# Performance work log

Measured on AMD Instinct MI355X. Metric: run time of the kernel, lower is better.

Reference implementation:

```python
import jax, jax.numpy as jnp
import numpy as np
import math

B, S, D, H = 2, 2048, 1024, 16
HD = D // H  # head_dim = 64


def setup_inputs() -> dict:
    key = jax.random.key(0)
    k1, k2, k3, k4, k5 = jax.random.split(key, 5)
    scale_in = 1.0 / math.sqrt(D)
    return {
        "x": jax.random.normal(k1, (B, S, D), dtype=jnp.float32),
        "Wqkv": jax.random.normal(k2, (3 * D, D), dtype=jnp.float32) * scale_in,
        "bqkv": jax.random.normal(k3, (3 * D,), dtype=jnp.float32) * 0.01,
        "Wout": jax.random.normal(k4, (D, D), dtype=jnp.float32) * scale_in,
        "bout": jax.random.normal(k5, (D,), dtype=jnp.float32) * 0.01,
    }


def reference(x, Wqkv, bqkv, Wout, bout):
    Bs, Sl, Dm = x.shape
    # qkv projection: torch Linear is x @ W.T + b
    qkv = x @ Wqkv.T + bqkv                        # [B,S,3D]
    qkv = qkv.reshape(Bs, Sl, 3, H, HD)
    q, k, v = qkv[:, :, 0], qkv[:, :, 1], qkv[:, :, 2]  # each [B,S,H,d]
    softmax_scale = 1.0 / math.sqrt(HD)
    # NOTE: source einsum 'bshd,btjd->bsht' sums k over its head axis j.
    # Equivalent efficient form: pre-sum k (and v) over heads.
    k_sum = k.sum(axis=2)                          # [B,S,d]
    v_sum = v.sum(axis=2)                          # [B,S,d]
    scores = jnp.einsum('bshd,btd->bsht', q, k_sum) * softmax_scale  # [B,S,H,T]
    causal_mask = jnp.triu(jnp.ones((Sl, Sl), dtype=bool), k=1)      # [S,T]
    scores = jnp.where(causal_mask[None, :, None, :], -jnp.inf, scores)
    attn = jax.nn.softmax(scores, axis=-1)
    # dropout p=0.0 / eval mode -> identity
    out = jnp.einsum('bsht,btd->bshd', attn, v_sum)  # [B,S,H,d]
    out = out.reshape(Bs, Sl, Dm)
    return out @ Wout.T + bout
```

## Files before the change

kernel.cpp:

```cpp
#include <hip/hip_runtime.h>


#define S_LEN 2048
#define DIM 1024

using floatx4 = __attribute__((ext_vector_type(4))) float;
using halfx8  = __attribute__((ext_vector_type(8))) _Float16;
using halfx4  = __attribute__((ext_vector_type(4))) _Float16;

__device__ __forceinline__ floatx4 mfma16(halfx8 a, halfx8 b, floatx4 c) {
  return __builtin_amdgcn_mfma_f32_16x16x32_f16(a, b, c, 0, 0, 0);
}

__device__ __forceinline__ void gll16(const void* g, void* l) {
  __builtin_amdgcn_global_load_lds(
      (const __attribute__((address_space(1))) void*)g,
      (__attribute__((address_space(3))) void*)l, 16, 0, 0);
}

__global__ __launch_bounds__(256) void prep_all(
    const float* __restrict__ x, const float* __restrict__ wqkv,
    const float* __restrict__ bqkv, const float* __restrict__ wout,
    _Float16* __restrict__ xb, _Float16* __restrict__ wcomb,
    _Float16* __restrict__ woutb, float* __restrict__ bcomb) {
  int bx = blockIdx.x;
  if (bx < 6144) {
    size_t i4 = ((size_t)bx * 256 + threadIdx.x) * 4;
    const float* src;
    _Float16* dst;
    size_t off;
    if (i4 < 4194304) { src = x; dst = xb; off = i4; }
    else if (i4 < 5242880) { src = wqkv; dst = wcomb; off = i4 - 4194304; }
    else { src = wout; dst = woutb; off = i4 - 5242880; }
    float4 v = *(const float4*)(src + off);
    halfx4 o;
    o[0] = (_Float16)v.x; o[1] = (_Float16)v.y;
    o[2] = (_Float16)v.z; o[3] = (_Float16)v.w;
    *(halfx4*)(dst + off) = o;
  } else {
    int gid = (bx - 6144) * 256 + threadIdx.x;
    int c = gid >> 10, j = gid & 1023;
    int row0 = (c < 64) ? (1024 + c) : (2048 + c - 64);
    float s = 0.f;
#pragma unroll
    for (int h = 0; h < 16; ++h) s += wqkv[(size_t)(row0 + h * 64) * 1024 + j];
    wcomb[(size_t)1024 * 1024 + gid] = (_Float16)s;
    if (gid < 1024) bcomb[gid] = bqkv[gid];
    if (gid < 128) {
      int b0 = (gid < 64) ? (1024 + gid) : (2048 + gid - 64);
      float sb = 0.f;
#pragma unroll
      for (int h = 0; h < 16; ++h) sb += bqkv[b0 + h * 64];
      bcomb[1024 + gid] = sb;
    }
  }
}

template <int MODE>
__global__ __launch_bounds__(256, 2) void gemm_t2(
    const _Float16* __restrict__ A, const _Float16* __restrict__ W,
    const float* __restrict__ bias, void* __restrict__ Cv,
    _Float16* __restrict__ kbo, _Float16* __restrict__ vto) {
  const int K = 1024;
  __shared__ _Float16 As[128][64];
  __shared__ _Float16 Ws[128][64];
  int tid = threadIdx.x;
  int lane = tid & 63, w = tid >> 6, ln = lane & 15, q4 = lane >> 4;
  int m0 = blockIdx.x * 128, n0 = blockIdx.y * 128;
  int mh = (w & 1) * 64, nh = (w >> 1) * 64;
  int rr = lane >> 3, gg = ((lane & 7) ^ rr) * 8;
  const _Float16* agp = A + (size_t)(m0 + w * 32 + rr) * K + gg;
  const _Float16* wgp = W + (size_t)(n0 + w * 32 + rr) * K + gg;
  floatx4 acc[4][4] = {};
  for (int kt = 0; kt < K; kt += 64) {
    __syncthreads();
#pragma unroll
    for (int j = 0; j < 4; ++j) {
      gll16(agp + (size_t)(8 * j) * K + kt, &As[w * 32 + 8 * j][0]);
      gll16(wgp + (size_t)(8 * j) * K + kt, &Ws[w * 32 + 8 * j][0]);
    }
    __syncthreads();
#pragma unroll
    for (int kh = 0; kh < 2; ++kh) {
      int sw = ((q4 + 4 * kh) ^ (ln & 7)) * 8;
      halfx8 bf[4];
#pragma unroll
      for (int nf = 0; nf < 4; ++nf)
        bf[nf] = *(const halfx8*)&Ws[nh + nf * 16 + ln][sw];
#pragma unroll
      for (int mf = 0; mf < 4; ++mf) {
        halfx8 af = *(const halfx8*)&As[mh + mf * 16 + ln][sw];
#pragma unroll
        for (int nf = 0; nf < 4; ++nf)
          acc[mf][nf] = mfma16(af, bf[nf], acc[mf][nf]);
      }
    }
  }
  const float qscale = 0.18033688011112042f;
#pragma unroll
  for (int nf = 0; nf < 4; ++nf) {
    int col = n0 + nh + nf * 16 + ln;
    float bv = bias[col];
    if constexpr (MODE == 1) {
#pragma unroll
      for (int mf = 0; mf < 4; ++mf)
#pragma unroll
        for (int i = 0; i < 4; ++i) {
          int row = m0 + mh + mf * 16 + q4 * 4 + i;
          ((float*)Cv)[(size_t)row * 1024 + col] = acc[mf][nf][i] + bv;
        }
    } else {
      if (col < 1024) {
#pragma unroll
        for (int mf = 0; mf < 4; ++mf)
#pragma unroll
          for (int i = 0; i < 4; ++i) {
            int row = m0 + mh + mf * 16 + q4 * 4 + i;
            ((_Float16*)Cv)[(size_t)row * 1024 + col] =
                (_Float16)((acc[mf][nf][i] + bv) * qscale);
          }
      } else if (col < 1088) {
        int ck = col - 1024;
#pragma unroll
        for (int mf = 0; mf < 4; ++mf)
#pragma unroll
          for (int i = 0; i < 4; ++i) {
            int row = m0 + mh + mf * 16 + q4 * 4 + i;
            kbo[(size_t)row * 64 + ck] = (_Float16)(acc[mf][nf][i] + bv);
          }
      } else {
        int d = col - 1088;
#pragma unroll
        for (int mf = 0; mf < 4; ++mf) {
          int row0 = m0 + mh + mf * 16 + q4 * 4;
          int bb = row0 >> 11, sps = row0 & 2047;
          halfx4 o;
#pragma unroll
          for (int i = 0; i < 4; ++i) o[i] = (_Float16)(acc[mf][nf][i] + bv);
          *(halfx4*)&vto[((size_t)((bb << 6) + d)) * S_LEN + sps] = o;
        }
      }
    }
  }
}

__global__ __launch_bounds__(256, 4) void flash_attn7(
    const _Float16* __restrict__ Qb, const _Float16* __restrict__ kb,
    const _Float16* __restrict__ vtb, _Float16* __restrict__ aob) {
  __shared__ _Float16 Ks[128][64];
  __shared__ _Float16 Vt[64][128];
  __shared__ _Float16 Ps[4][16][72];
  int tid = threadIdx.x;
  int lane = tid & 63, w = tid >> 6, ln = lane & 15, q4 = lane >> 4;
  int idx = 1023 - (int)blockIdx.x;
  int c = idx >> 1, b = idx & 1;
  int s0 = c * 4;
  int s = s0 + w;
  size_t bS = (size_t)b * S_LEN;

  const _Float16* qp = Qb + (bS + s) * DIM + ln * 64 + q4 * 8;
  halfx8 bq0 = *(const halfx8*)qp, bq1 = *(const halfx8*)(qp + 32);

  float m_run = -1e30f, l_run = 0.f;
  floatx4 oacc[4] = {};

  int rr = lane >> 3, ggk = ((lane & 7) ^ rr) * 8;
  const _Float16* kgp = kb + (bS + w * 32 + rr) * 64 + ggk;
  int vrow = (lane >> 4);
  int vhalf = (lane >> 3) & 1, vg = lane & 7;
  const _Float16* vgp[4];
#pragma unroll
  for (int j = 0; j < 4; ++j) {
    int row = w * 16 + 4 * j + vrow;
    vgp[j] = vtb + ((size_t)b * 64 + row) * S_LEN + vhalf * 64 +
             ((vg ^ (row & 7)) * 8);
  }
  int swk0 = (q4 ^ (ln & 7)) * 8;
  int swk1 = ((q4 + 4) ^ (ln & 7)) * 8;
  _Float16* Pw = &Ps[w][0][0];
  int nt = (s0 >> 7) + 1;

  for (int it = 0; it < nt; ++it) {
    int t0 = it << 7;
    __syncthreads();
#pragma unroll
    for (int j = 0; j < 4; ++j) {
      gll16(kgp + (size_t)(t0 + 8 * j) * 64, &Ks[w * 32 + 8 * j][0]);
      gll16(vgp[j] + t0, &Vt[w * 16 + 4 * j][0]);
    }
    __syncthreads();

#pragma unroll
    for (int tq = 0; tq < 2; ++tq) {
      int t0q = t0 + tq * 64;
      if (t0q > s) break;
      floatx4 sf[4];
#pragma unroll
      for (int tf = 0; tf < 4; ++tf) {
        halfx8 ak0 = *(const halfx8*)&Ks[tq * 64 + tf * 16 + ln][swk0];
        halfx8 ak1 = *(const halfx8*)&Ks[tq * 64 + tf * 16 + ln][swk1];
        floatx4 z = {};
        z = mfma16(ak0, bq0, z);
        sf[tf] = mfma16(ak1, bq1, z);
      }
      if (t0q + 63 > s) {
#pragma unroll
        for (int tf = 0; tf < 4; ++tf)
#pragma unroll
          for (int i = 0; i < 4; ++i) {
            int t = t0q + tf * 16 + q4 * 4 + i;
            if (t > s) sf[tf][i] = -1e30f;
          }
      }
      float tm = fmaxf(fmaxf(sf[0][0], sf[0][1]), fmaxf(sf[0][2], sf[0][3]));
#pragma unroll
      for (int tf = 1; tf < 4; ++tf)
        tm = fmaxf(tm, fmaxf(fmaxf(sf[tf][0], sf[tf][1]),
                             fmaxf(sf[tf][2], sf[tf][3])));
      tm = fmaxf(tm, __shfl_xor(tm, 16));
      tm = fmaxf(tm, __shfl_xor(tm, 32));
      float mn = fmaxf(m_run, tm);
      float alpha = exp2f(m_run - mn);
      m_run = mn;
      float rs = 0.f;
#pragma unroll
      for (int tf = 0; tf < 4; ++tf) {
        float p0 = exp2f(sf[tf][0] - mn), p1 = exp2f(sf[tf][1] - mn);
        float p2 = exp2f(sf[tf][2] - mn), p3 = exp2f(sf[tf][3] - mn);
        rs += (p0 + p1) + (p2 + p3);
        halfx4 pk;
        pk[0] = (_Float16)p0; pk[1] = (_Float16)p1;
        pk[2] = (_Float16)p2; pk[3] = (_Float16)p3;
        *(halfx4*)&Pw[ln * 72 + tf * 16 + q4 * 4] = pk;
      }
      rs += __shfl_xor(rs, 16);
      rs += __shfl_xor(rs, 32);
      l_run = l_run * alpha + rs;
      halfx8 bp0 = *(const halfx8*)&Pw[ln * 72 + q4 * 8];
      halfx8 bp1 = *(const halfx8*)&Pw[ln * 72 + 32 + q4 * 8];
#pragma unroll
      for (int n2 = 0; n2 < 4; ++n2) {
        halfx8 av0 = *(const halfx8*)&Vt[n2 * 16 + ln][tq * 64 + swk0];
        halfx8 av1 = *(const halfx8*)&Vt[n2 * 16 + ln][tq * 64 + swk1];
#pragma unroll
        for (int i = 0; i < 4; ++i) oacc[n2][i] *= alpha;
        oacc[n2] = mfma16(av0, bp0, oacc[n2]);
        oacc[n2] = mfma16(av1, bp1, oacc[n2]);
      }
    }
  }
  float inv = 1.0f / l_run;
#pragma unroll
  for (int n2 = 0; n2 < 4; ++n2) {
    halfx4 o;
#pragma unroll
    for (int i = 0; i < 4; ++i) o[i] = (_Float16)(oacc[n2][i] * inv);
    *(halfx4*)(aob + (bS + s) * DIM + ln * 64 + n2 * 16 + q4 * 4) = o;
  }
}

extern "C" void kernel_launch(void* const* d_in, const int* in_sizes, int n_in,
                              void* d_out, int out_size, void* d_ws,
                              size_t ws_size, hipStream_t stream) {
  const float* x    = (const float*)d_in[0];
  const float* wqkv = (const float*)d_in[1];
  const float* bqkv = (const float*)d_in[2];
  const float* wout = (const float*)d_in[3];
  const float* bout = (const float*)d_in[4];
  float* out = (float*)d_out;
  char* ws = (char*)d_ws;
  _Float16* xb    = (_Float16*)(ws);
  _Float16* qb    = (_Float16*)(ws + (8u << 20));
  _Float16* aob   = (_Float16*)(ws + (16u << 20));
  _Float16* kb    = (_Float16*)(ws + (24u << 20));
  _Float16* vtb   = (_Float16*)(ws + (24u << 20) + (512u << 10));
  _Float16* wcomb = (_Float16*)(ws + (25u << 20));
  _Float16* woutb = (_Float16*)(ws + (27u << 20) + (512u << 10));
  float*    bcomb = (float*)(ws + (29u << 20) + (512u << 10));

  hipLaunchKernelGGL(prep_all, dim3(6656), dim3(256), 0, stream,
                     x, wqkv, bqkv, wout, xb, wcomb, woutb, bcomb);
  hipLaunchKernelGGL((gemm_t2<0>), dim3(32, 9), dim3(256), 0, stream,
                     xb, wcomb, bcomb, (void*)qb, kb, vtb);
  hipLaunchKernelGGL(flash_attn7, dim3(1024), dim3(256), 0, stream,
                     qb, kb, vtb, aob);
  hipLaunchKernelGGL((gemm_t2<1>), dim3(32, 8), dim3(256), 0, stream,
                     aob, woutb, bout, (void*)out, nullptr, nullptr);
}
```

Baseline: 169.0 us.

## Split KV tile across two wave groups with split-softmax merge in flash attention

Doubles the attention block to 512 threads. Two groups of four waves each process one 64-key half of every 128-key tile for the same four query rows, and their partial outputs, maxes and sums are merged through shared memory at the end. It also skips rescaling the accumulator unless the running max grows by more than a threshold, and raises wave priority around the MFMA sections. The aim is more parallelism per block and less serial softmax work, at the cost of an extra reduction pass and more threads sitting idle on causal tiles.

```diff
diff --git a/kernel.cpp b/kernel.cpp
--- a/kernel.cpp
+++ b/kernel.cpp
@@ -144,18 +144,19 @@
   }
 }
 
-__global__ __launch_bounds__(256, 4) void flash_attn7(
+__global__ __launch_bounds__(512, 6) void flash_attn8(
     const _Float16* __restrict__ Qb, const _Float16* __restrict__ kb,
     const _Float16* __restrict__ vtb, _Float16* __restrict__ aob) {
   __shared__ _Float16 Ks[128][64];
   __shared__ _Float16 Vt[64][128];
-  __shared__ _Float16 Ps[4][16][72];
+  __shared__ _Float16 Ps[8][16][72];
   int tid = threadIdx.x;
   int lane = tid & 63, w = tid >> 6, ln = lane & 15, q4 = lane >> 4;
+  int g = w >> 2;
   int idx = 1023 - (int)blockIdx.x;
   int c = idx >> 1, b = idx & 1;
   int s0 = c * 4;
-  int s = s0 + w;
+  int s = s0 + (w & 3);
   size_t bS = (size_t)b * S_LEN;
 
   const _Float16* qp = Qb + (bS + s) * DIM + ln * 64 + q4 * 8;
@@ -165,13 +166,13 @@
   floatx4 oacc[4] = {};
 
   int rr = lane >> 3, ggk = ((lane & 7) ^ rr) * 8;
-  const _Float16* kgp = kb + (bS + w * 32 + rr) * 64 + ggk;
-  int vrow = (lane >> 4);
+  const _Float16* kgp = kb + (bS + w * 16 + rr) * 64 + ggk;
+  int vr = lane >> 4;
   int vhalf = (lane >> 3) & 1, vg = lane & 7;
-  const _Float16* vgp[4];
-#pragma unroll
-  for (int j = 0; j < 4; ++j) {
-    int row = w * 16 + 4 * j + vrow;
+  const _Float16* vgp[2];
+#pragma unroll
+  for (int j = 0; j < 2; ++j) {
+    int row = w * 8 + 4 * j + vr;
     vgp[j] = vtb + ((size_t)b * 64 + row) * S_LEN + vhalf * 64 +
              ((vg ^ (row & 7)) * 8);
   }
@@ -184,25 +185,25 @@
     int t0 = it << 7;
     __syncthreads();
 #pragma unroll
-    for (int j = 0; j < 4; ++j) {
-      gll16(kgp + (size_t)(t0 + 8 * j) * 64, &Ks[w * 32 + 8 * j][0]);
-      gll16(vgp[j] + t0, &Vt[w * 16 + 4 * j][0]);
+    for (int j = 0; j < 2; ++j) {
+      gll16(kgp + (size_t)(t0 + 8 * j) * 64, &Ks[w * 16 + 8 * j][0]);
+      gll16(vgp[j] + t0, &Vt[w * 8 + 4 * j][0]);
     }
     __syncthreads();
 
-#pragma unroll
-    for (int tq = 0; tq < 2; ++tq) {
-      int t0q = t0 + tq * 64;
-      if (t0q > s) break;
+    int t0q = t0 + (g << 6);
+    if (t0q <= s) {
       floatx4 sf[4];
+      __builtin_amdgcn_s_setprio(1);
 #pragma unroll
       for (int tf = 0; tf < 4; ++tf) {
-        halfx8 ak0 = *(const halfx8*)&Ks[tq * 64 + tf * 16 + ln][swk0];
-        halfx8 ak1 = *(const halfx8*)&Ks[tq * 64 + tf * 16 + ln][swk1];
+        halfx8 ak0 = *(const halfx8*)&Ks[(g << 6) + tf * 16 + ln][swk0];
+        halfx8 ak1 = *(const halfx8*)&Ks[(g << 6) + tf * 16 + ln][swk1];
         floatx4 z = {};
         z = mfma16(ak0, bq0, z);
         sf[tf] = mfma16(ak1, bq1, z);
       }
+      __builtin_amdgcn_s_setprio(0);
       if (t0q + 63 > s) {
 #pragma unroll
         for (int tf = 0; tf < 4; ++tf)
@@ -219,14 +220,21 @@
                              fmaxf(sf[tf][2], sf[tf][3])));
       tm = fmaxf(tm, __shfl_xor(tm, 16));
       tm = fmaxf(tm, __shfl_xor(tm, 32));
-      float mn = fmaxf(m_run, tm);
-      float alpha = exp2f(m_run - mn);
-      m_run = mn;
+      if (!__all(tm <= m_run + 8.f)) {
+        float mn = fmaxf(m_run, tm);
+        float alpha = exp2f(m_run - mn);
+        m_run = mn;
+        l_run *= alpha;
+#pragma unroll
+        for (int n2 = 0; n2 < 4; ++n2)
+#pragma unroll
+          for (int i = 0; i < 4; ++i) oacc[n2][i] *= alpha;
+      }
       float rs = 0.f;
 #pragma unroll
       for (int tf = 0; tf < 4; ++tf) {
-        float p0 = exp2f(sf[tf][0] - mn), p1 = exp2f(sf[tf][1] - mn);
-        float p2 = exp2f(sf[tf][2] - mn), p3 = exp2f(sf[tf][3] - mn);
+        float p0 = exp2f(sf[tf][0] - m_run), p1 = exp2f(sf[tf][1] - m_run);
+        float p2 = exp2f(sf[tf][2] - m_run), p3 = exp2f(sf[tf][3] - m_run);
         rs += (p0 + p1) + (p2 + p3);
         halfx4 pk;
         pk[0] = (_Float16)p0; pk[1] = (_Float16)p1;
@@ -235,27 +243,47 @@
       }
       rs += __shfl_xor(rs, 16);
       rs += __shfl_xor(rs, 32);
-      l_run = l_run * alpha + rs;
+      l_run += rs;
       halfx8 bp0 = *(const halfx8*)&Pw[ln * 72 + q4 * 8];
       halfx8 bp1 = *(const halfx8*)&Pw[ln * 72 + 32 + q4 * 8];
+      __builtin_amdgcn_s_setprio(1);
 #pragma unroll
       for (int n2 = 0; n2 < 4; ++n2) {
-        halfx8 av0 = *(const halfx8*)&Vt[n2 * 16 + ln][tq * 64 + swk0];
-        halfx8 av1 = *(const halfx8*)&Vt[n2 * 16 + ln][tq * 64 + swk1];
-#pragma unroll
-        for (int i = 0; i < 4; ++i) oacc[n2][i] *= alpha;
+        halfx8 av0 = *(const halfx8*)&Vt[n2 * 16 + ln][(g << 6) + swk0];
+        halfx8 av1 = *(const halfx8*)&Vt[n2 * 16 + ln][(g << 6) + swk1];
         oacc[n2] = mfma16(av0, bp0, oacc[n2]);
         oacc[n2] = mfma16(av1, bp1, oacc[n2]);
       }
-    }
-  }
-  float inv = 1.0f / l_run;
-#pragma unroll
-  for (int n2 = 0; n2 < 4; ++n2) {
-    halfx4 o;
-#pragma unroll
-    for (int i = 0; i < 4; ++i) o[i] = (_Float16)(oacc[n2][i] * inv);
-    *(halfx4*)(aob + (bS + s) * DIM + ln * 64 + n2 * 16 + q4 * 4) = o;
+      __builtin_amdgcn_s_setprio(0);
+    }
+  }
+
+  __syncthreads();
+  if (g == 1) {
+    float* sb = (float*)&Ps[(w & 3) * 2][0][0];
+#pragma unroll
+    for (int n2 = 0; n2 < 4; ++n2)
+#pragma unroll
+      for (int i = 0; i < 4; ++i) sb[(n2 * 4 + i) * 64 + lane] = oacc[n2][i];
+    sb[1024 + lane] = m_run;
+    sb[1088 + lane] = l_run;
+  }
+  __syncthreads();
+  if (g == 0) {
+    float* sb = (float*)&Ps[w * 2][0][0];
+    float m2 = sb[1024 + lane], l2 = sb[1088 + lane];
+    float mn = fmaxf(m_run, m2);
+    float a1 = exp2f(m_run - mn), a2 = exp2f(m2 - mn);
+    float linv = 1.0f / (l_run * a1 + l2 * a2);
+#pragma unroll
+    for (int n2 = 0; n2 < 4; ++n2) {
+      halfx4 o;
+#pragma unroll
+      for (int i = 0; i < 4; ++i)
+        o[i] = (_Float16)((oacc[n2][i] * a1 + sb[(n2 * 4 + i) * 64 + lane] * a2) *
+                          linv);
+      *(halfx4*)(aob + (bS + s) * DIM + ln * 64 + n2 * 16 + q4 * 4) = o;
+    }
   }
 }
 
@@ -282,7 +310,7 @@
                      x, wqkv, bqkv, wout, xb, wcomb, woutb, bcomb);
   hipLaunchKernelGGL((gemm_t2<0>), dim3(32, 9), dim3(256), 0, stream,
                      xb, wcomb, bcomb, (void*)qb, kb, vtb);
-  hipLaunchKernelGGL(flash_attn7, dim3(1024), dim3(256), 0, stream,
+  hipLaunchKernelGGL(flash_attn8, dim3(1024), dim3(512), 0, stream,
                      qb, kb, vtb, aob);
   hipLaunchKernelGGL((gemm_t2<1>), dim3(32, 8), dim3(256), 0, stream,
                      aob, woutb, bout, (void*)out, nullptr, nullptr);
```

After: 166.5 us. About the same (-1.5%).

## Restructure flash attention with 8-wave blocks, paired causal tiles, lazy rescale

Applied to the files above, without the earlier changes.

The attention kernel now uses 512-thread blocks of 8 waves, so each K/V tile load is shared by twice as many query rows. Each block handles two query chunks, a low one and its mirrored high one, to balance causal work across blocks. The softmax max and rescale now run once per 128-key tile and are skipped when the new max stays within a threshold. The P layout is reorganised for wider MFMA operand reads, and s_setprio hints are added around the MFMA sections. This aims to cut redundant K/V loads, load imbalance and rescale cost, at the price of more LDS per block and a possible drop in occupancy.

```diff
diff --git a/kernel.cpp b/kernel.cpp
--- a/kernel.cpp
+++ b/kernel.cpp
@@ -144,118 +144,142 @@
   }
 }
 
-__global__ __launch_bounds__(256, 4) void flash_attn7(
+__global__ __launch_bounds__(512, 4) void flash_attn10(
     const _Float16* __restrict__ Qb, const _Float16* __restrict__ kb,
     const _Float16* __restrict__ vtb, _Float16* __restrict__ aob) {
   __shared__ _Float16 Ks[128][64];
   __shared__ _Float16 Vt[64][128];
-  __shared__ _Float16 Ps[4][16][72];
+  __shared__ _Float16 Ps[8][2048];
   int tid = threadIdx.x;
   int lane = tid & 63, w = tid >> 6, ln = lane & 15, q4 = lane >> 4;
-  int idx = 1023 - (int)blockIdx.x;
-  int c = idx >> 1, b = idx & 1;
-  int s0 = c * 4;
-  int s = s0 + w;
+  int bx = (int)blockIdx.x;
+  int p = bx >> 1, b = bx & 1;
   size_t bS = (size_t)b * S_LEN;
 
-  const _Float16* qp = Qb + (bS + s) * DIM + ln * 64 + q4 * 8;
-  halfx8 bq0 = *(const halfx8*)qp, bq1 = *(const halfx8*)(qp + 32);
-
-  float m_run = -1e30f, l_run = 0.f;
-  floatx4 oacc[4] = {};
-
   int rr = lane >> 3, ggk = ((lane & 7) ^ rr) * 8;
-  const _Float16* kgp = kb + (bS + w * 32 + rr) * 64 + ggk;
-  int vrow = (lane >> 4);
+  const _Float16* kgp = kb + (bS + w * 16 + rr) * 64 + ggk;
+  int vr = lane >> 4;
   int vhalf = (lane >> 3) & 1, vg = lane & 7;
-  const _Float16* vgp[4];
-#pragma unroll
-  for (int j = 0; j < 4; ++j) {
-    int row = w * 16 + 4 * j + vrow;
+  const _Float16* vgp[2];
+#pragma unroll
+  for (int j = 0; j < 2; ++j) {
+    int row = w * 8 + 4 * j + vr;
     vgp[j] = vtb + ((size_t)b * 64 + row) * S_LEN + vhalf * 64 +
              ((vg ^ (row & 7)) * 8);
   }
   int swk0 = (q4 ^ (ln & 7)) * 8;
   int swk1 = ((q4 + 4) ^ (ln & 7)) * 8;
-  _Float16* Pw = &Ps[w][0][0];
-  int nt = (s0 >> 7) + 1;
-
-  for (int it = 0; it < nt; ++it) {
-    int t0 = it << 7;
-    __syncthreads();
-#pragma unroll
-    for (int j = 0; j < 4; ++j) {
-      gll16(kgp + (size_t)(t0 + 8 * j) * 64, &Ks[w * 32 + 8 * j][0]);
-      gll16(vgp[j] + t0, &Vt[w * 16 + 4 * j][0]);
-    }
-    __syncthreads();
-
-#pragma unroll
-    for (int tq = 0; tq < 2; ++tq) {
-      int t0q = t0 + tq * 64;
-      if (t0q > s) break;
-      floatx4 sf[4];
-#pragma unroll
-      for (int tf = 0; tf < 4; ++tf) {
-        halfx8 ak0 = *(const halfx8*)&Ks[tq * 64 + tf * 16 + ln][swk0];
-        halfx8 ak1 = *(const halfx8*)&Ks[tq * 64 + tf * 16 + ln][swk1];
-        floatx4 z = {};
-        z = mfma16(ak0, bq0, z);
-        sf[tf] = mfma16(ak1, bq1, z);
-      }
-      if (t0q + 63 > s) {
+  _Float16* Pw = &Ps[w][0];
+  int pwbase = (q4 >> 1) * 128 + ln * 8 + (q4 & 1) * 4;
+  int prbase = q4 * 128 + ln * 8;
+
+  for (int pass = 0; pass < 2; ++pass) {
+    int c = pass ? (255 - p) : p;
+    int s0 = c * 8;
+    int s = s0 + w;
+
+    const _Float16* qp = Qb + (bS + s) * DIM + ln * 64 + q4 * 8;
+    halfx8 bq0 = *(const halfx8*)qp, bq1 = *(const halfx8*)(qp + 32);
+
+    float m_run = -1e30f, l_run = 0.f;
+    floatx4 oacc[4] = {};
+    int nt = (c >> 4) + 1;
+
+    for (int it = 0; it < nt; ++it) {
+      int t0 = it << 7;
+      __syncthreads();
+      gll16(kgp + (size_t)t0 * 64, &Ks[w * 16][0]);
+      gll16(kgp + (size_t)(t0 + 8) * 64, &Ks[w * 16 + 8][0]);
+      gll16(vgp[0] + t0, &Vt[w * 8][0]);
+      gll16(vgp[1] + t0, &Vt[w * 8 + 4][0]);
+      __syncthreads();
+
+      floatx4 sf[2][4];
+      __builtin_amdgcn_s_setprio(1);
+#pragma unroll
+      for (int tq = 0; tq < 2; ++tq)
+#pragma unroll
+        for (int tf = 0; tf < 4; ++tf) {
+          halfx8 ak0 = *(const halfx8*)&Ks[tq * 64 + tf * 16 + ln][swk0];
+          halfx8 ak1 = *(const halfx8*)&Ks[tq * 64 + tf * 16 + ln][swk1];
+          floatx4 z = {};
+          z = mfma16(ak0, bq0, z);
+          sf[tq][tf] = mfma16(ak1, bq1, z);
+        }
+      __builtin_amdgcn_s_setprio(0);
+      if (it == nt - 1) {
+#pragma unroll
+        for (int tq = 0; tq < 2; ++tq)
+#pragma unroll
+          for (int tf = 0; tf < 4; ++tf)
+#pragma unroll
+            for (int i = 0; i < 4; ++i) {
+              int t = t0 + tq * 64 + tf * 16 + q4 * 4 + i;
+              if (t > s) sf[tq][tf][i] = -1e30f;
+            }
+      }
+      float tm = -1e30f;
+#pragma unroll
+      for (int tq = 0; tq < 2; ++tq)
 #pragma unroll
         for (int tf = 0; tf < 4; ++tf)
-#pragma unroll
-          for (int i = 0; i < 4; ++i) {
-            int t = t0q + tf * 16 + q4 * 4 + i;
-            if (t > s) sf[tf][i] = -1e30f;
-          }
-      }
-      float tm = fmaxf(fmaxf(sf[0][0], sf[0][1]), fmaxf(sf[0][2], sf[0][3]));
-#pragma unroll
-      for (int tf = 1; tf < 4; ++tf)
-        tm = fmaxf(tm, fmaxf(fmaxf(sf[tf][0], sf[tf][1]),
-                             fmaxf(sf[tf][2], sf[tf][3])));
+          tm = fmaxf(tm, fmaxf(fmaxf(sf[tq][tf][0], sf[tq][tf][1]),
+                               fmaxf(sf[tq][tf][2], sf[tq][tf][3])));
       tm = fmaxf(tm, __shfl_xor(tm, 16));
       tm = fmaxf(tm, __shfl_xor(tm, 32));
-      float mn = fmaxf(m_run, tm);
-      float alpha = exp2f(m_run - mn);
-      m_run = mn;
+      if (!__all(tm <= m_run + 8.f)) {
+        float mn = fmaxf(m_run, tm);
+        float alpha = exp2f(m_run - mn);
+        m_run = mn;
+        l_run *= alpha;
+#pragma unroll
+        for (int n2 = 0; n2 < 4; ++n2)
+#pragma unroll
+          for (int i = 0; i < 4; ++i) oacc[n2][i] *= alpha;
+      }
       float rs = 0.f;
 #pragma unroll
-      for (int tf = 0; tf < 4; ++tf) {
-        float p0 = exp2f(sf[tf][0] - mn), p1 = exp2f(sf[tf][1] - mn);
-        float p2 = exp2f(sf[tf][2] - mn), p3 = exp2f(sf[tf][3] - mn);
-        rs += (p0 + p1) + (p2 + p3);
-        halfx4 pk;
-        pk[0] = (_Float16)p0; pk[1] = (_Float16)p1;
-        pk[2] = (_Float16)p2; pk[3] = (_Float16)p3;
-        *(halfx4*)&Pw[ln * 72 + tf * 16 + q4 * 4] = pk;
-      }
+      for (int tq = 0; tq < 2; ++tq)
+#pragma unroll
+        for (int tf = 0; tf < 4; ++tf) {
+          float p0 = exp2f(sf[tq][tf][0] - m_run);
+          float p1 = exp2f(sf[tq][tf][1] - m_run);
+          float p2 = exp2f(sf[tq][tf][2] - m_run);
+          float p3 = exp2f(sf[tq][tf][3] - m_run);
+          rs += (p0 + p1) + (p2 + p3);
+          halfx4 pk;
+          pk[0] = (_Float16)p0; pk[1] = (_Float16)p1;
+          pk[2] = (_Float16)p2; pk[3] = (_Float16)p3;
+          *(halfx4*)&Pw[(tq * 8 + tf * 2) * 128 + pwbase] = pk;
+        }
       rs += __shfl_xor(rs, 16);
       rs += __shfl_xor(rs, 32);
-      l_run = l_run * alpha + rs;
-      halfx8 bp0 = *(const halfx8*)&Pw[ln * 72 + q4 * 8];
-      halfx8 bp1 = *(const halfx8*)&Pw[ln * 72 + 32 + q4 * 8];
-#pragma unroll
-      for (int n2 = 0; n2 < 4; ++n2) {
-        halfx8 av0 = *(const halfx8*)&Vt[n2 * 16 + ln][tq * 64 + swk0];
-        halfx8 av1 = *(const halfx8*)&Vt[n2 * 16 + ln][tq * 64 + swk1];
-#pragma unroll
-        for (int i = 0; i < 4; ++i) oacc[n2][i] *= alpha;
-        oacc[n2] = mfma16(av0, bp0, oacc[n2]);
-        oacc[n2] = mfma16(av1, bp1, oacc[n2]);
-      }
-    }
-  }
-  float inv = 1.0f / l_run;
-#pragma unroll
-  for (int n2 = 0; n2 < 4; ++n2) {
-    halfx4 o;
-#pragma unroll
-    for (int i = 0; i < 4; ++i) o[i] = (_Float16)(oacc[n2][i] * inv);
-    *(halfx4*)(aob + (bS + s) * DIM + ln * 64 + n2 * 16 + q4 * 4) = o;
+      l_run += rs;
+      halfx8 bp[4];
+#pragma unroll
+      for (int kc = 0; kc < 4; ++kc)
+        bp[kc] = *(const halfx8*)&Pw[kc * 512 + prbase];
+      __builtin_amdgcn_s_setprio(1);
+#pragma unroll
+      for (int kc = 0; kc < 4; ++kc) {
+        int half = (kc >> 1) * 64;
+        int sw = ((q4 + 4 * (kc & 1)) ^ (ln & 7)) * 8;
+#pragma unroll
+        for (int n2 = 0; n2 < 4; ++n2) {
+          halfx8 av = *(const halfx8*)&Vt[n2 * 16 + ln][half + sw];
+          oacc[n2] = mfma16(av, bp[kc], oacc[n2]);
+        }
+      }
+      __builtin_amdgcn_s_setprio(0);
+    }
+    float inv = 1.0f / l_run;
+#pragma unroll
+    for (int n2 = 0; n2 < 4; ++n2) {
+      halfx4 o;
+#pragma unroll
+      for (int i = 0; i < 4; ++i) o[i] = (_Float16)(oacc[n2][i] * inv);
+      *(halfx4*)(aob + (bS + s) * DIM + ln * 64 + n2 * 16 + q4 * 4) = o;
+    }
   }
 }
 
@@ -282,7 +306,7 @@
                      x, wqkv, bqkv, wout, xb, wcomb, woutb, bcomb);
   hipLaunchKernelGGL((gemm_t2<0>), dim3(32, 9), dim3(256), 0, stream,
                      xb, wcomb, bcomb, (void*)qb, kb, vtb);
-  hipLaunchKernelGGL(flash_attn7, dim3(1024), dim3(256), 0, stream,
+  hipLaunchKernelGGL(flash_attn10, dim3(512), dim3(512), 0, stream,
                      qb, kb, vtb, aob);
   hipLaunchKernelGGL((gemm_t2<1>), dim3(32, 8), dim3(256), 0, stream,
                      aob, woutb, bout, (void*)out, nullptr, nullptr);
```

Result: slower. 195.6 us (+15.7%).
